# Performance work log

Measured on AMD Instinct MI355X. Metric: run time of the kernel, lower is better.

## Reference

```python
import jax, jax.numpy as jnp
import numpy as np

B, K, N, DIM, C_IN = 4, 2048, 4096, 3, 61
IN = DIM + C_IN        # 64, deepset input size
H1, H2 = 128, 128      # neighbor_xf hidden sizes
OUT = 64               # c_out // heads
HEADS = 4
EPS = 1e-5             # BatchNorm eps


def _lin(key, i, o):
    return jax.random.normal(key, (i, o), jnp.float32) * (1.0 / np.sqrt(i))


def setup_inputs() -> dict:
    key = jax.random.key(0)
    ks = jax.random.split(key, 12)
    return {
        "keys": jax.random.normal(ks[0], (B, K, DIM), jnp.float32),
        "points": jax.random.normal(ks[1], (B, N, DIM), jnp.float32),
        "feats": jax.random.normal(ks[2], (B, N, C_IN), jnp.float32),
        "nx_w1": _lin(ks[3], IN, H1), "nx_b1": jnp.zeros((H1,), jnp.float32),
        "nx_w2": _lin(ks[4], H1, H2), "nx_b2": jnp.zeros((H2,), jnp.float32),
        "nx_w3": _lin(ks[5], H2, OUT), "nx_b3": jnp.zeros((OUT,), jnp.float32),
        "sx_w1": _lin(ks[6], IN, IN), "sx_b1": jnp.zeros((IN,), jnp.float32),
        "sx_w2": _lin(ks[7], IN, IN), "sx_b2": jnp.zeros((IN,), jnp.float32),
        "sx_w3": _lin(ks[8], IN, IN), "sx_b3": jnp.zeros((IN,), jnp.float32),
        "att_w": _lin(ks[9], 2 * IN, HEADS * IN),
        "att_b": jnp.zeros((HEADS * IN,), jnp.float32),
        "att_q": jax.random.normal(ks[10], (HEADS, IN), jnp.float32) * 0.1,
        "bn_gamma": jnp.ones((IN,), jnp.float32),
        "bn_beta": jnp.zeros((IN,), jnp.float32),
        "neighbors": 32,
    }


def _mlp3(x, w1, b1, w2, b2, w3, b3):
    # per-element deepset MLP: Linear-ReLU-Linear-ReLU-Linear
    h = jax.nn.relu(x @ w1 + b1)
    h = jax.nn.relu(h @ w2 + b2)
    return h @ w3 + b3


def _forward(keys, points, feats, nx_w1, nx_b1, nx_w2, nx_b2, nx_w3, nx_b3,
             sx_w1, sx_b1, sx_w2, sx_b2, sx_w3, sx_b3,
             att_w, att_b, att_q, bn_gamma, bn_beta, neighbors):
    b = keys.shape[0]
    # Euclidean dist_fn: dist_vec [B,K,N,dim], dist [B,K,N], all points valid
    rel = points[:, None, :, :] - keys[:, :, None, :]
    dist = jnp.sqrt(jnp.sum(rel * rel, axis=-1))
    _, idx = jax.lax.top_k(-dist, neighbors)                   # [B,K,k] nearest
    nrel = jnp.take_along_axis(rel, idx[..., None], axis=2)    # [B,K,k,dim]
    bidx = jnp.arange(b)[:, None, None]
    nfeat = feats[bidx, idx]                                   # [B,K,k,c_in]
    comb = jnp.concatenate([nrel, nfeat], axis=-1)             # [B,K,k,in]
    lat = _mlp3(comb, nx_w1, nx_b1, nx_w2, nx_b2, nx_w3, nx_b3)  # [B,K,k,out]
    # BatchNorm1d (training-mode batch stats) over flattened [B*K*k, in]
    flat = comb.reshape(-1, comb.shape[-1])
    mean = jnp.mean(flat, axis=0)
    var = jnp.var(flat, axis=0)
    norm = (comb - mean) * jax.lax.rsqrt(var + EPS) * bn_gamma + bn_beta
    # SelfAttention: deepset sum-pooled context + per-neighbor softmax weights
    set_feat = jnp.sum(_mlp3(norm, sx_w1, sx_b1, sx_w2, sx_b2, sx_w3, sx_b3), axis=2)
    comb_feat = jnp.concatenate(
        [norm, jnp.broadcast_to(set_feat[:, :, None, :], norm.shape)], axis=-1)
    heads = (comb_feat @ att_w + att_b).reshape(comb_feat.shape[:3] + (HEADS, -1))
    e = jnp.sum(heads * att_q, axis=-1)                        # [B,K,k,H]
    w = jax.nn.softmax(e, axis=-2)                             # softmax over neighbor axis
    out = jnp.einsum('bkno,bknh->bkoh', lat, w)                # weighted reduce over k
    return out.reshape(out.shape[:2] + (-1,))                  # [B,K,out*H]


def reference(keys, points, feats, nx_w1, nx_b1, nx_w2, nx_b2, nx_w3, nx_b3,
              sx_w1, sx_b1, sx_w2, sx_b2, sx_w3, sx_b3,
              att_w, att_b, att_q, bn_gamma, bn_beta, neighbors):
    return _forward(keys, points, feats, nx_w1, nx_b1, nx_w2, nx_b2, nx_w3, nx_b3,
                    sx_w1, sx_b1, sx_w2, sx_b2, sx_w3, sx_b3,
                    att_w, att_b, att_q, bn_gamma, bn_beta, neighbors)
```

## Files before the change

kernel.cpp:

```cpp
#include <hip/hip_runtime.h>
#include <math.h>

#define BATCH 4
#define KQ    2048
#define NPTS  4096
#define CIN   61
#define KNN   32
#define ROWS  (BATCH*KQ*KNN)

#define OFF_IDX  0
#define OFF_ACC  524288
#define OFF_ATTA 557056
#define OFF_W1F  558080
#define OFF_W2F  574464
#define OFF_W3F  607232

typedef __attribute__((ext_vector_type(8)))  short bfrag;
typedef __attribute__((ext_vector_type(16))) float cfrag;

__device__ __forceinline__ unsigned short bf16_rne(float x) {
  unsigned u = __float_as_uint(x);
  unsigned r = u + 0x7fffu + ((u >> 16) & 1u);
  return (unsigned short)(r >> 16);
}
__device__ __forceinline__ float4 ld4u(const float* p) {
  float4 r; __builtin_memcpy(&r, p, 16); return r;
}

#define NCAND 320

template<int NS>
__device__ __forceinline__ void select_emit(
    const unsigned* __restrict__ VAL, const int* __restrict__ IDXL,
    int mcount, unsigned hib, unsigned lob, int lane,
    const float* __restrict__ Pb, float kx, float ky, float kz,
    unsigned short* __restrict__ dst, int* __restrict__ SEL,
    float* __restrict__ accs) {
  const unsigned long long lmask = (1ull << lane) - 1ull;
  unsigned e[NS];
#pragma unroll
  for (int s = 0; s < NS; ++s) {
    int ei = s*64 + lane;
    e[s] = (ei < mcount) ? VAL[ei] : 0xffffffffu;
  }
  unsigned lo2 = lob, hi2 = hib;
  while (lo2 < hi2) {
    unsigned mid = lo2 + ((hi2 - lo2) >> 1);
    int c = 0;
#pragma unroll
    for (int s = 0; s < NS; ++s) c += (int)__popcll(__ballot(e[s] <= mid));
    if (c == KNN) { hi2 = mid; break; }
    if (c > KNN) hi2 = mid; else lo2 = mid + 1;
  }
  const unsigned T = hi2;
  float r0=0.f,r1=0.f,r2=0.f,r3=0.f,r4=0.f,r5=0.f;
  int base2 = 0;
#pragma unroll
  for (int s = 0; s < NS; ++s) {
    bool p = (e[s] <= T);
    unsigned long long m = __ballot(p);
    if (p) {
      int pos = base2 + (int)__popcll(m & lmask);
      if (pos < KNN) {
        int n = IDXL[s*64 + lane];
        SEL[pos] = n;
        dst[pos] = (unsigned short)n;
        float dx = Pb[n*3+0]-kx, dy = Pb[n*3+1]-ky, dz = Pb[n*3+2]-kz;
        r0 += dx; r1 += dy; r2 += dz;
        r3 += dx*dx; r4 += dy*dy; r5 += dz*dz;
      }
    }
    base2 += (int)__popcll(m);
  }
#pragma unroll
  for (int off = 32; off > 0; off >>= 1) {
    r0 += __shfl_down(r0, off); r1 += __shfl_down(r1, off);
    r2 += __shfl_down(r2, off); r3 += __shfl_down(r3, off);
    r4 += __shfl_down(r4, off); r5 += __shfl_down(r5, off);
  }
  if (lane == 0) {
    atomicAdd(&accs[0], r0); atomicAdd(&accs[1], r1); atomicAdd(&accs[2], r2);
    atomicAdd(&accs[64], r3); atomicAdd(&accs[65], r4); atomicAdd(&accs[66], r5);
  }
}

__device__ __forceinline__ void dispatch_select(
    const unsigned* VAL, const int* IDXL, int mcount, unsigned hib, unsigned lob,
    int lane, const float* Pb, float kx, float ky, float kz,
    unsigned short* dst, int* SEL, float* accs) {
  if (mcount <= 64)
    select_emit<1>(VAL, IDXL, mcount, hib, lob, lane, Pb, kx, ky, kz, dst, SEL, accs);
  else if (mcount <= 128)
    select_emit<2>(VAL, IDXL, mcount, hib, lob, lane, Pb, kx, ky, kz, dst, SEL, accs);
  else
    select_emit<5>(VAL, IDXL, mcount, hib, lob, lane, Pb, kx, ky, kz, dst, SEL, accs);
}

__global__ __launch_bounds__(256, 6) void topk_kernel(
    const float* __restrict__ keys, const float* __restrict__ points,
    const float* __restrict__ feats,
    const float* __restrict__ w1, const float* __restrict__ w2,
    const float* __restrict__ w3,
    const float* __restrict__ att_w, const float* __restrict__ att_q,
    unsigned short* __restrict__ idx_out, float* __restrict__ acc,
    short* __restrict__ w1f, short* __restrict__ w2f, short* __restrict__ w3f,
    float* __restrict__ attA) {
  if (blockIdx.x >= 4096) {
    const int bb = blockIdx.x - 4096;
    if (bb == 128) {
      const int t = threadIdx.x, c = t >> 2, h = t & 3;
      float s = 0.f;
      for (int d = 0; d < 64; ++d) s += att_w[c*256 + h*64 + d] * att_q[h*64 + d];
      attA[c*4 + h] = s;
      return;
    }
    int t = bb * 256 + threadIdx.x;
    if (t < 8192) {
      int j = t & 7, lane = (t >> 3) & 63, tk = t >> 9;
      int kc = tk & 3, tile = tk >> 2;
      int nh = tile*32 + (lane & 31), k = kc*16 + (lane >> 5)*8 + j;
      w1f[t] = (short)bf16_rne(w1[k*128 + nh]);
    } else if (t < 24576) {
      int t2 = t - 8192;
      int j = t2 & 7, lane = (t2 >> 3) & 63, tk = t2 >> 9;
      int kc = tk & 7, tile = tk >> 3;
      int nh = tile*32 + (lane & 31), k = kc*16 + (lane >> 5)*8 + j;
      w2f[t2] = (short)bf16_rne(w2[k*128 + nh]);
    } else {
      int t3 = t - 24576;
      int j = t3 & 7, lane = (t3 >> 3) & 63, tk = t3 >> 9;
      int kc = tk & 7, tile = tk >> 3;
      int nh = tile*32 + (lane & 31), k = kc*16 + (lane >> 5)*8 + j;
      w3f[t3] = (short)bf16_rne(w3[k*64 + nh]);
    }
    return;
  }

  __shared__ unsigned VAL[2][NCAND];
  __shared__ int IDXL[2][NCAND];
  __shared__ int SEL[2][KNN];
  __shared__ unsigned HIW[2][4], LOW[2][4];
  __shared__ int WTOT[2][4];
  __shared__ float FRED[64*33];
  __shared__ float FQ[64*33];
  const int tid = threadIdx.x;
  const int lane = tid & 63, wid = tid >> 6;
  const int g0 = blockIdx.x * 2, g1 = g0 + 1;
  const int b = g0 >> 11;
  const float kxA = keys[(size_t)g0*3+0], kyA = keys[(size_t)g0*3+1], kzA = keys[(size_t)g0*3+2];
  const float kxB = keys[(size_t)g1*3+0], kyB = keys[(size_t)g1*3+1], kzB = keys[(size_t)g1*3+2];
  const float* __restrict__ Pb = points + (size_t)b * NPTS * 3;

  unsigned uA[16], uB[16];
  unsigned lminA = 0xffffffffu, lminB = 0xffffffffu;
#pragma unroll
  for (int c4 = 0; c4 < 4; ++c4) {
    const float* pp = Pb + (size_t)(tid*16 + c4*4) * 3;
    float4 A = ld4u(pp), B4 = ld4u(pp + 4), C4 = ld4u(pp + 8);
    float x, y, z, dx, dy, dz;
#define DPT(slot, PX, PY, PZ)                                        \
    x = PX; y = PY; z = PZ;                                          \
    dx = x-kxA; dy = y-kyA; dz = z-kzA;                              \
    uA[slot] = __float_as_uint(dx*dx + dy*dy + dz*dz);               \
    lminA = min(lminA, uA[slot]);                                    \
    dx = x-kxB; dy = y-kyB; dz = z-kzB;                              \
    uB[slot] = __float_as_uint(dx*dx + dy*dy + dz*dz);               \
    lminB = min(lminB, uB[slot]);
    DPT(c4*4+0, A.x,  A.y,  A.z)
    DPT(c4*4+1, A.w,  B4.x, B4.y)
    DPT(c4*4+2, B4.z, B4.w, C4.x)
    DPT(c4*4+3, C4.y, C4.z, C4.w)
#undef DPT
  }
  unsigned wloA = lminA, whiA = lminA, wloB = lminB, whiB = lminB;
#pragma unroll
  for (int off = 1; off < 64; off <<= 1) {
    unsigned a0 = (unsigned)__shfl_xor((int)wloA, off);
    unsigned a1 = (unsigned)__shfl_xor((int)whiA, off);
    unsigned b0 = (unsigned)__shfl_xor((int)wloB, off);
    unsigned b1 = (unsigned)__shfl_xor((int)whiB, off);
    wloA = min(wloA, a0); whiA = max(whiA, a1);
    wloB = min(wloB, b0); whiB = max(whiB, b1);
  }
  unsigned hiA, hiB;
  {
    unsigned lo = wloA, hi = whiA;
    while (lo < hi) {
      unsigned mid = lo + ((hi - lo) >> 1);
      int c = (int)__popcll(__ballot(lminA <= mid));
      if (c == KNN) { hi = mid; break; }
      if (c > KNN) hi = mid; else lo = mid + 1;
    }
    hiA = hi;
    lo = wloB; hi = whiB;
    while (lo < hi) {
      unsigned mid = lo + ((hi - lo) >> 1);
      int c = (int)__popcll(__ballot(lminB <= mid));
      if (c == KNN) { hi = mid; break; }
      if (c > KNN) hi = mid; else lo = mid + 1;
    }
    hiB = hi;
  }
  if (lane == 0) {
    HIW[0][wid] = hiA; HIW[1][wid] = hiB;
    LOW[0][wid] = wloA; LOW[1][wid] = wloB;
  }
  __syncthreads();
  const unsigned hibA = min(min(HIW[0][0],HIW[0][1]), min(HIW[0][2],HIW[0][3]));
  const unsigned hibB = min(min(HIW[1][0],HIW[1][1]), min(HIW[1][2],HIW[1][3]));
  const unsigned lobA = min(min(LOW[0][0],LOW[0][1]), min(LOW[0][2],LOW[0][3]));
  const unsigned lobB = min(min(LOW[1][0],LOW[1][1]), min(LOW[1][2],LOW[1][3]));

  int cntA = 0, cntB = 0;
#pragma unroll
  for (int j = 0; j < 16; ++j) {
    cntA += (uA[j] <= hibA) ? 1 : 0;
    cntB += (uB[j] <= hibB) ? 1 : 0;
  }
  int incA = cntA, incB = cntB;
#pragma unroll
  for (int off = 1; off < 64; off <<= 1) {
    int tA = __shfl_up(incA, off);
    int tB = __shfl_up(incB, off);
    if (lane >= off) { incA += tA; incB += tB; }
  }
  if (lane == 63) { WTOT[0][wid] = incA; WTOT[1][wid] = incB; }
  __syncthreads();
  int baseA = incA - cntA, baseB = incB - cntB;
  for (int w = 0; w < wid; ++w) { baseA += WTOT[0][w]; baseB += WTOT[1][w]; }
  {
    int pA = baseA, pB = baseB;
#pragma unroll
    for (int j = 0; j < 16; ++j) {
      if (uA[j] <= hibA) {
        if (pA < NCAND) { VAL[0][pA] = uA[j]; IDXL[0][pA] = tid*16 + j; }
        ++pA;
      }
      if (uB[j] <= hibB) {
        if (pB < NCAND) { VAL[1][pB] = uB[j]; IDXL[1][pB] = tid*16 + j; }
        ++pB;
      }
    }
  }
  __syncthreads();
  const int mcountA = min(WTOT[0][0]+WTOT[0][1]+WTOT[0][2]+WTOT[0][3], NCAND);
  const int mcountB = min(WTOT[1][0]+WTOT[1][1]+WTOT[1][2]+WTOT[1][3], NCAND);

  float* accs = &acc[(blockIdx.x & 63)*128];
  if (wid == 0) {
    dispatch_select(VAL[0], IDXL[0], mcountA, hibA, lobA, lane, Pb,
                    kxA, kyA, kzA, idx_out + (size_t)g0*KNN, SEL[0], accs);
  } else if (wid == 2) {
    dispatch_select(VAL[1], IDXL[1], mcountB, hibB, lobB, lane, Pb,
                    kxB, kyB, kzB, idx_out + (size_t)g1*KNN, SEL[1], accs);
  }
  __syncthreads();

  {
    const int row = tid >> 3, chunk = tid & 7;
    const int nA = SEL[0][row], nB = SEL[1][row];
    const float* frA = feats + ((size_t)b*NPTS + nA)*CIN;
    const float* frB = feats + ((size_t)b*NPTS + nB)*CIN;
    float fs[8] = {0,0,0,0,0,0,0,0}, fq[8] = {0,0,0,0,0,0,0,0};
    if (chunk < 7) {
      float4 a0 = ld4u(frA + chunk*8), a1 = ld4u(frA + chunk*8 + 4);
      float4 b0 = ld4u(frB + chunk*8), b1 = ld4u(frB + chunk*8 + 4);
      fs[0]=a0.x+b0.x; fq[0]=a0.x*a0.x+b0.x*b0.x;
      fs[1]=a0.y+b0.y; fq[1]=a0.y*a0.y+b0.y*b0.y;
      fs[2]=a0.z+b0.z; fq[2]=a0.z*a0.z+b0.z*b0.z;
      fs[3]=a0.w+b0.w; fq[3]=a0.w*a0.w+b0.w*b0.w;
      fs[4]=a1.x+b1.x; fq[4]=a1.x*a1.x+b1.x*b1.x;
      fs[5]=a1.y+b1.y; fq[5]=a1.y*a1.y+b1.y*b1.y;
      fs[6]=a1.z+b1.z; fq[6]=a1.z*a1.z+b1.z*b1.z;
      fs[7]=a1.w+b1.w; fq[7]=a1.w*a1.w+b1.w*b1.w;
    } else {
#pragma unroll
      for (int i = 0; i < 5; ++i) {
        float va = frA[56+i], vb = frB[56+i];
        fs[i] = va + vb; fq[i] = va*va + vb*vb;
      }
    }
#pragma unroll
    for (int i = 0; i < 8; ++i) {
      FRED[(chunk*8 + i)*33 + row] = fs[i];
      FQ  [(chunk*8 + i)*33 + row] = fq[i];
    }
  }
  __syncthreads();
  if (tid < 64) {
    float s = 0.f, q2 = 0.f;
#pragma unroll
    for (int r = 0; r < 32; ++r) {
      s  += FRED[tid*33 + r];
      q2 += FQ[tid*33 + r];
    }
    if (tid < CIN) {
      atomicAdd(&accs[3 + tid], s);
      atomicAdd(&accs[64 + 3 + tid], q2);
    }
  }
}

#define L_W1F 0
#define L_W2F 16384
#define L_W3F 49152
#define L_B1  65536
#define L_B2  66048
#define L_B3  66560
#define L_AE  66816
#define L_ACT 67840
#define L_EPX 137472
#define L_TOT 145664

template<int KC, bool F32OUT>
__device__ __forceinline__ void gemm_part(const short* WF,
    const float* BIAS, short* ACTq, float* LATq,
    const bfrag* B, int tile0, int ntiles, int m, int q, int lane) {
#pragma unroll
  for (int t = 0; t < ntiles; ++t) {
    const int tile = tile0 + t;
    cfrag acc;
#pragma unroll
    for (int i = 0; i < 16; ++i) acc[i] = 0.f;
#pragma unroll
    for (int kc = 0; kc < KC; ++kc) {
      bfrag a = *(const bfrag*)(WF + ((tile*KC + kc)*64 + lane)*8);
      acc = __builtin_amdgcn_mfma_f32_32x32x16_bf16(a, B[kc], acc, 0, 0, 0);
    }
#pragma unroll
    for (int p = 0; p < 4; ++p) {
      const int nh = tile*32 + p*8 + q*4;
      float4 bv = *(const float4*)(BIAS + nh);
      if (F32OUT) {
        float4 o;
        o.x = acc[4*p+0] + bv.x; o.y = acc[4*p+1] + bv.y;
        o.z = acc[4*p+2] + bv.z; o.w = acc[4*p+3] + bv.w;
        *(float4*)(LATq + m*68 + nh) = o;
      } else {
        short4 s;
        s.x = (short)bf16_rne(fmaxf(acc[4*p+0] + bv.x, 0.f));
        s.y = (short)bf16_rne(fmaxf(acc[4*p+1] + bv.y, 0.f));
        s.z = (short)bf16_rne(fmaxf(acc[4*p+2] + bv.z, 0.f));
        s.w = (short)bf16_rne(fmaxf(acc[4*p+3] + bv.w, 0.f));
        *(short4*)(ACTq + m*136 + nh) = s;
      }
    }
  }
}

__global__ __launch_bounds__(1024, 4) void main_kernel(
    const float* __restrict__ keys, const float* __restrict__ points,
    const float* __restrict__ feats, const unsigned short* __restrict__ idxg,
    const short* __restrict__ w1f, const short* __restrict__ w2f,
    const short* __restrict__ w3f,
    const float* __restrict__ b1, const float* __restrict__ b2,
    const float* __restrict__ b3,
    const float* __restrict__ attAg, const float* __restrict__ accg,
    const float* __restrict__ gammav, float* __restrict__ out) {
  __shared__ __align__(16) char smem[L_TOT];
  const int tid = threadIdx.x;
  const int bid = blockIdx.x;
  const int wid = tid >> 6, lane = tid & 63;
  const int pairq = wid >> 1, wv = wid & 1;
  const int m = lane & 31, q = lane >> 5;

  short* SW1 = (short*)(smem + L_W1F);
  short* SW2 = (short*)(smem + L_W2F);
  short* SW3 = (short*)(smem + L_W3F);
  float* SB1 = (float*)(smem + L_B1);
  float* SB2 = (float*)(smem + L_B2);
  float* SB3 = (float*)(smem + L_B3);
  float* SAe = (float*)(smem + L_AE);
  short* ACTq = (short*)(smem + L_ACT + pairq * 8704);
  float* LATq = (float*)(smem + L_ACT + pairq * 8704);
  float* EPX  = (float*)(smem + L_EPX) + pairq * 256;

  {
    ((uint4*)SW1)[tid] = ((const uint4*)w1f)[tid];
    ((uint4*)SW2)[tid] = ((const uint4*)w2f)[tid];
    ((uint4*)SW2)[tid + 1024] = ((const uint4*)w2f)[tid + 1024];
    ((uint4*)SW3)[tid] = ((const uint4*)w3f)[tid];
    if (tid < 128) SB1[tid] = b1[tid];
    else if (tid < 256) SB2[tid-128] = b2[tid-128];
    else if (tid < 320) SB3[tid-256] = b3[tid-256];
    float* TMP = (float*)(smem + L_ACT);
    if (tid < 512) {
      int c = tid & 63, p = tid >> 6;
      float s = 0.f, s2 = 0.f;
      for (int k = p; k < 64; k += 8) {
        s += accg[k*128 + c]; s2 += accg[k*128 + 64 + c];
      }
      TMP[p*128 + c] = s; TMP[p*128 + 64 + c] = s2;
    }
    __syncthreads();
    float* SCt = (float*)(smem + L_EPX);
    if (tid < 64) {
      float s = 0.f, s2 = 0.f;
#pragma unroll
      for (int p = 0; p < 8; ++p) { s += TMP[p*128 + tid]; s2 += TMP[p*128 + 64 + tid]; }
      const float invR = 1.f / (float)ROWS;
      float mean = s * invR;
      float var = s2 * invR - mean * mean;
      SCt[tid] = gammav[tid] * rsqrtf(var + 1e-5f);
    }
    __syncthreads();
    if (tid < 256) SAe[tid] = attAg[tid] * SCt[tid >> 2];
    __syncthreads();
  }

  auto load_gather = [&](int grp2, float* v) {
    const int g2 = grp2 * 8 + pairq;
    const int bq2 = g2 >> 11;
    const int c0 = wv*32 + q*16;
    const int n = (int)idxg[(size_t)g2*KNN + m];
    const float* frow = feats + ((size_t)bq2*NPTS + n)*CIN;
    if (wv == 0 && q == 0) {
      const float* Pb = points + (size_t)bq2 * NPTS * 3;
      v[0] = Pb[n*3+0] - keys[(size_t)g2*3+0];
      v[1] = Pb[n*3+1] - keys[(size_t)g2*3+1];
      v[2] = Pb[n*3+2] - keys[(size_t)g2*3+2];
#pragma unroll
      for (int kk = 0; kk < 3; ++kk) {
        float4 t = ld4u(frow + kk*4);
        v[3+kk*4+0] = t.x; v[3+kk*4+1] = t.y; v[3+kk*4+2] = t.z; v[3+kk*4+3] = t.w;
      }
      v[15] = frow[12];
    } else {
      const int base = c0 - 3;
#pragma unroll
      for (int kk = 0; kk < 4; ++kk) {
        float4 t = ld4u(frow + base + kk*4);
        v[kk*4+0] = t.x; v[kk*4+1] = t.y; v[kk*4+2] = t.z; v[kk*4+3] = t.w;
      }
    }
  };

  float vcur[16];
  load_gather(bid, vcur);

  for (int grp = bid; grp < BATCH*KQ/8; grp += 256) {
    const int g = grp * 8 + pairq;
    const int c0 = wv*32 + q*16;

    {
      float ep0 = 0.f, ep1 = 0.f, ep2 = 0.f, ep3 = 0.f;
#pragma unroll
      for (int cc = 0; cc < 16; ++cc) {
        float4 ae = *(const float4*)(SAe + (c0 + cc)*4);
        ep0 = fmaf(vcur[cc], ae.x, ep0);
        ep1 = fmaf(vcur[cc], ae.y, ep1);
        ep2 = fmaf(vcur[cc], ae.z, ep2);
        ep3 = fmaf(vcur[cc], ae.w, ep3);
      }
      ep0 += __shfl_xor(ep0, 32); ep1 += __shfl_xor(ep1, 32);
      ep2 += __shfl_xor(ep2, 32); ep3 += __shfl_xor(ep3, 32);
#pragma unroll
      for (int k = 0; k < 2; ++k) {
        bfrag pk;
#pragma unroll
        for (int t = 0; t < 8; ++t) pk[t] = (short)bf16_rne(vcur[k*8 + t]);
        *(bfrag*)(ACTq + m*136 + c0 + k*8) = pk;
      }
      if (q == 0) {
        float4 e4; e4.x = ep0; e4.y = ep1; e4.z = ep2; e4.w = ep3;
        *(float4*)(EPX + m*8 + wv*4) = e4;
      }
    }
    __syncthreads();

    float vnext[16];
    const int gnext = grp + 256;
    if (gnext < BATCH*KQ/8) load_gather(gnext, vnext);

    if (wv == 0) {
      const int h0 = q*2;
      float ea = EPX[m*8 + h0]     + EPX[m*8 + 4 + h0];
      float eb = EPX[m*8 + h0 + 1] + EPX[m*8 + 5 + h0];
      float ma = ea, mb = eb;
#pragma unroll
      for (int off = 1; off < 32; off <<= 1) {
        ma = fmaxf(ma, __shfl_xor(ma, off));
        mb = fmaxf(mb, __shfl_xor(mb, off));
      }
      float xa = __expf(ea - ma), xb = __expf(eb - mb);
      float sa = xa, sb = xb;
#pragma unroll
      for (int off = 1; off < 32; off <<= 1) {
        sa += __shfl_xor(sa, off);
        sb += __shfl_xor(sb, off);
      }
      EPX[m*8 + h0]     = xa / sa;
      EPX[m*8 + h0 + 1] = xb / sb;
    }

    {
      bfrag B4[4];
#pragma unroll
      for (int kc = 0; kc < 4; ++kc)
        B4[kc] = *(const bfrag*)(ACTq + m*136 + kc*16 + q*8);
      __syncthreads();
      gemm_part<4, false>(SW1, SB1, ACTq, LATq, B4, wv*2, 2, m, q, lane);
    }
    __syncthreads();
    {
      bfrag B8[8];
#pragma unroll
      for (int kc = 0; kc < 8; ++kc)
        B8[kc] = *(const bfrag*)(ACTq + m*136 + kc*16 + q*8);
      __syncthreads();
      gemm_part<8, false>(SW2, SB2, ACTq, LATq, B8, wv*2, 2, m, q, lane);
    }
    __syncthreads();
    {
      bfrag C8[8];
#pragma unroll
      for (int kc = 0; kc < 8; ++kc)
        C8[kc] = *(const bfrag*)(ACTq + m*136 + kc*16 + q*8);
      __syncthreads();
      gemm_part<8, true>(SW3, SB3, ACTq, LATq, C8, wv, 1, m, q, lane);
    }
    __syncthreads();

    {
      const int oi = wv*64 + lane;
      const int o = oi >> 1, hp = oi & 1;
      float a0 = 0.f, a1 = 0.f;
#pragma unroll
      for (int n2 = 0; n2 < KNN; ++n2) {
        float l = LATq[n2*68 + o];
        float2 wv2 = *(const float2*)(EPX + n2*8 + hp*2);
        a0 = fmaf(l, wv2.x, a0);
        a1 = fmaf(l, wv2.y, a1);
      }
      float2 r; r.x = a0; r.y = a1;
      *(float2*)(out + (size_t)g*256 + o*4 + hp*2) = r;
    }
    __syncthreads();

#pragma unroll
    for (int i = 0; i < 16; ++i) vcur[i] = vnext[i];
  }
}

extern "C" void kernel_launch(void* const* d_in, const int* in_sizes, int n_in,
                              void* d_out, int out_size, void* d_ws, size_t ws_size,
                              hipStream_t stream) {
  const float* keys   = (const float*)d_in[0];
  const float* points = (const float*)d_in[1];
  const float* feats  = (const float*)d_in[2];
  const float* nx_w1  = (const float*)d_in[3];
  const float* nx_b1  = (const float*)d_in[4];
  const float* nx_w2  = (const float*)d_in[5];
  const float* nx_b2  = (const float*)d_in[6];
  const float* nx_w3  = (const float*)d_in[7];
  const float* nx_b3  = (const float*)d_in[8];
  const float* att_w  = (const float*)d_in[15];
  const float* att_q  = (const float*)d_in[17];
  const float* gamma  = (const float*)d_in[18];
  float* out = (float*)d_out;

  char* ws = (char*)d_ws;
  unsigned short* idxp = (unsigned short*)(ws + OFF_IDX);
  float* acc  = (float*)(ws + OFF_ACC);
  float* attA = (float*)(ws + OFF_ATTA);
  short* w1f  = (short*)(ws + OFF_W1F);
  short* w2f  = (short*)(ws + OFF_W2F);
  short* w3f  = (short*)(ws + OFF_W3F);

  hipMemsetAsync(acc, 0, 32768, stream);
  topk_kernel<<<4096 + 129, 256, 0, stream>>>(keys, points, feats,
      nx_w1, nx_w2, nx_w3, att_w, att_q, idxp, acc, w1f, w2f, w3f, attA);
  main_kernel<<<256, 1024, 0, stream>>>(keys, points, feats, idxp,
      w1f, w2f, w3f, nx_b1, nx_b2, nx_b3, attA, acc, gamma, out);
}
```

Baseline: 183.3 us.

## Keep MLP activations in MFMA registers and compute attention logits and pooling via MFMA

The main kernel is restructured so each wavefront handles one query group entirely in registers. Layer outputs are repacked directly as the next MFMA operand, which needs reordered weight fragment layouts for w2/w3. The attention logits and the weighted neighbor reduction now run as split-precision (hi/lo bf16) MFMAs instead of scalar FMA loops and shared-memory staging. This removes most LDS round-trips and block-wide barriers and shrinks shared memory, changing the launch to 512 blocks of 512 threads. The trade-offs are higher register pressure and extra MFMAs to keep near-fp32 accuracy on the softmax and pooling.

Result: faster. 167.1 us (-8.9%).

```diff
diff --git a/kernel.cpp b/kernel.cpp
--- a/kernel.cpp
+++ b/kernel.cpp
@@ -16,6 +16,7 @@
 #define OFF_W3F  607232
 
 typedef __attribute__((ext_vector_type(8)))  short bfrag;
+typedef __attribute__((ext_vector_type(4)))  unsigned ufrag;
 typedef __attribute__((ext_vector_type(16))) float cfrag;
 
 __device__ __forceinline__ unsigned short bf16_rne(float x) {
@@ -25,6 +26,29 @@
 }
 __device__ __forceinline__ float4 ld4u(const float* p) {
   float4 r; __builtin_memcpy(&r, p, 16); return r;
+}
+__device__ __forceinline__ unsigned cvtpk(float lo, float hi) {
+  unsigned r;
+  asm("v_cvt_pk_bf16_f32 %0, %1, %2" : "=v"(r) : "v"(lo), "v"(hi));
+  return r;
+}
+__device__ __forceinline__ float up_lo(unsigned pk) { return __uint_as_float(pk << 16); }
+__device__ __forceinline__ float up_hi(unsigned pk) { return __uint_as_float(pk & 0xffff0000u); }
+
+__device__ __forceinline__ cfrag zero16() {
+  cfrag z;
+#pragma unroll
+  for (int i = 0; i < 16; ++i) z[i] = 0.f;
+  return z;
+}
+__device__ __forceinline__ cfrag mfma_bu(bfrag a, ufrag b, cfrag c) {
+  return __builtin_amdgcn_mfma_f32_32x32x16_bf16(a, __builtin_bit_cast(bfrag, b), c, 0, 0, 0);
+}
+__device__ __forceinline__ cfrag mfma_ub(ufrag a, bfrag b, cfrag c) {
+  return __builtin_amdgcn_mfma_f32_32x32x16_bf16(__builtin_bit_cast(bfrag, a), b, c, 0, 0, 0);
+}
+__device__ __forceinline__ cfrag mfma_uu(ufrag a, ufrag b, cfrag c) {
+  return __builtin_amdgcn_mfma_f32_32x32x16_bf16(__builtin_bit_cast(bfrag, a), __builtin_bit_cast(bfrag, b), c, 0, 0, 0);
 }
 
 #define NCAND 320
@@ -124,13 +148,15 @@
       int t2 = t - 8192;
       int j = t2 & 7, lane = (t2 >> 3) & 63, tk = t2 >> 9;
       int kc = tk & 7, tile = tk >> 3;
-      int nh = tile*32 + (lane & 31), k = kc*16 + (lane >> 5)*8 + j;
+      int nh = tile*32 + (lane & 31);
+      int k = 32*(kc>>1) + 16*(kc&1) + 4*(lane>>5) + (j&3) + 8*(j>>2);
       w2f[t2] = (short)bf16_rne(w2[k*128 + nh]);
     } else {
       int t3 = t - 24576;
       int j = t3 & 7, lane = (t3 >> 3) & 63, tk = t3 >> 9;
       int kc = tk & 7, tile = tk >> 3;
-      int nh = tile*32 + (lane & 31), k = kc*16 + (lane >> 5)*8 + j;
+      int nh = tile*32 + (lane & 31);
+      int k = 32*(kc>>1) + 16*(kc&1) + 4*(lane>>5) + (j&3) + 8*(j>>2);
       w3f[t3] = (short)bf16_rne(w3[k*64 + nh]);
     }
     return;
@@ -304,51 +330,16 @@
 #define L_W1F 0
 #define L_W2F 16384
 #define L_W3F 49152
-#define L_B1  65536
-#define L_B2  66048
-#define L_B3  66560
-#define L_AE  66816
-#define L_ACT 67840
-#define L_EPX 137472
-#define L_TOT 145664
-
-template<int KC, bool F32OUT>
-__device__ __forceinline__ void gemm_part(const short* WF,
-    const float* BIAS, short* ACTq, float* LATq,
-    const bfrag* B, int tile0, int ntiles, int m, int q, int lane) {
-#pragma unroll
-  for (int t = 0; t < ntiles; ++t) {
-    const int tile = tile0 + t;
-    cfrag acc;
-#pragma unroll
-    for (int i = 0; i < 16; ++i) acc[i] = 0.f;
-#pragma unroll
-    for (int kc = 0; kc < KC; ++kc) {
-      bfrag a = *(const bfrag*)(WF + ((tile*KC + kc)*64 + lane)*8);
-      acc = __builtin_amdgcn_mfma_f32_32x32x16_bf16(a, B[kc], acc, 0, 0, 0);
-    }
-#pragma unroll
-    for (int p = 0; p < 4; ++p) {
-      const int nh = tile*32 + p*8 + q*4;
-      float4 bv = *(const float4*)(BIAS + nh);
-      if (F32OUT) {
-        float4 o;
-        o.x = acc[4*p+0] + bv.x; o.y = acc[4*p+1] + bv.y;
-        o.z = acc[4*p+2] + bv.z; o.w = acc[4*p+3] + bv.w;
-        *(float4*)(LATq + m*68 + nh) = o;
-      } else {
-        short4 s;
-        s.x = (short)bf16_rne(fmaxf(acc[4*p+0] + bv.x, 0.f));
-        s.y = (short)bf16_rne(fmaxf(acc[4*p+1] + bv.y, 0.f));
-        s.z = (short)bf16_rne(fmaxf(acc[4*p+2] + bv.z, 0.f));
-        s.w = (short)bf16_rne(fmaxf(acc[4*p+3] + bv.w, 0.f));
-        *(short4*)(ACTq + m*136 + nh) = s;
-      }
-    }
-  }
-}
-
-__global__ __launch_bounds__(1024, 4) void main_kernel(
+#define L_SH  65536
+#define L_SL  69632
+#define L_B1  73728
+#define L_B2  74240
+#define L_B3  74752
+#define L_WSC 75008
+#define L_SC  79104
+#define L_TOT 79360
+
+__global__ __launch_bounds__(512, 4) void main_kernel(
     const float* __restrict__ keys, const float* __restrict__ points,
     const float* __restrict__ feats, const unsigned short* __restrict__ idxg,
     const short* __restrict__ w1f, const short* __restrict__ w2f,
@@ -361,30 +352,18 @@
   const int tid = threadIdx.x;
   const int bid = blockIdx.x;
   const int wid = tid >> 6, lane = tid & 63;
-  const int pairq = wid >> 1, wv = wid & 1;
-  const int m = lane & 31, q = lane >> 5;
-
-  short* SW1 = (short*)(smem + L_W1F);
-  short* SW2 = (short*)(smem + L_W2F);
-  short* SW3 = (short*)(smem + L_W3F);
-  float* SB1 = (float*)(smem + L_B1);
-  float* SB2 = (float*)(smem + L_B2);
-  float* SB3 = (float*)(smem + L_B3);
-  float* SAe = (float*)(smem + L_AE);
-  short* ACTq = (short*)(smem + L_ACT + pairq * 8704);
-  float* LATq = (float*)(smem + L_ACT + pairq * 8704);
-  float* EPX  = (float*)(smem + L_EPX) + pairq * 256;
+  const int col = lane & 31, h = lane >> 5;
 
   {
-    ((uint4*)SW1)[tid] = ((const uint4*)w1f)[tid];
-    ((uint4*)SW2)[tid] = ((const uint4*)w2f)[tid];
-    ((uint4*)SW2)[tid + 1024] = ((const uint4*)w2f)[tid + 1024];
-    ((uint4*)SW3)[tid] = ((const uint4*)w3f)[tid];
-    if (tid < 128) SB1[tid] = b1[tid];
-    else if (tid < 256) SB2[tid-128] = b2[tid-128];
-    else if (tid < 320) SB3[tid-256] = b3[tid-256];
-    float* TMP = (float*)(smem + L_ACT);
-    if (tid < 512) {
+    const uint4* src = (const uint4*)w1f;
+    uint4* dst = (uint4*)smem;
+#pragma unroll
+    for (int r = 0; r < 8; ++r) dst[r*512 + tid] = src[r*512 + tid];
+    if (tid < 128) ((float*)(smem + L_B1))[tid] = b1[tid];
+    else if (tid < 256) ((float*)(smem + L_B2))[tid-128] = b2[tid-128];
+    else if (tid < 320) ((float*)(smem + L_B3))[tid-256] = b3[tid-256];
+    float* TMP = (float*)(smem + L_WSC);
+    {
       int c = tid & 63, p = tid >> 6;
       float s = 0.f, s2 = 0.f;
       for (int k = p; k < 64; k += 8) {
@@ -393,7 +372,7 @@
       TMP[p*128 + c] = s; TMP[p*128 + 64 + c] = s2;
     }
     __syncthreads();
-    float* SCt = (float*)(smem + L_EPX);
+    float* SCp = (float*)(smem + L_SC);
     if (tid < 64) {
       float s = 0.f, s2 = 0.f;
 #pragma unroll
@@ -401,144 +380,193 @@
       const float invR = 1.f / (float)ROWS;
       float mean = s * invR;
       float var = s2 * invR - mean * mean;
-      SCt[tid] = gammav[tid] * rsqrtf(var + 1e-5f);
-    }
-    __syncthreads();
-    if (tid < 256) SAe[tid] = attAg[tid] * SCt[tid >> 2];
-    __syncthreads();
-  }
-
-  auto load_gather = [&](int grp2, float* v) {
-    const int g2 = grp2 * 8 + pairq;
-    const int bq2 = g2 >> 11;
-    const int c0 = wv*32 + q*16;
-    const int n = (int)idxg[(size_t)g2*KNN + m];
-    const float* frow = feats + ((size_t)bq2*NPTS + n)*CIN;
-    if (wv == 0 && q == 0) {
-      const float* Pb = points + (size_t)bq2 * NPTS * 3;
-      v[0] = Pb[n*3+0] - keys[(size_t)g2*3+0];
-      v[1] = Pb[n*3+1] - keys[(size_t)g2*3+1];
-      v[2] = Pb[n*3+2] - keys[(size_t)g2*3+2];
-#pragma unroll
-      for (int kk = 0; kk < 3; ++kk) {
-        float4 t = ld4u(frow + kk*4);
-        v[3+kk*4+0] = t.x; v[3+kk*4+1] = t.y; v[3+kk*4+2] = t.z; v[3+kk*4+3] = t.w;
-      }
-      v[15] = frow[12];
-    } else {
-      const int base = c0 - 3;
-#pragma unroll
-      for (int kk = 0; kk < 4; ++kk) {
-        float4 t = ld4u(frow + base + kk*4);
-        v[kk*4+0] = t.x; v[kk*4+1] = t.y; v[kk*4+2] = t.z; v[kk*4+3] = t.w;
-      }
-    }
-  };
-
-  float vcur[16];
-  load_gather(bid, vcur);
-
-  for (int grp = bid; grp < BATCH*KQ/8; grp += 256) {
-    const int g = grp * 8 + pairq;
-    const int c0 = wv*32 + q*16;
-
-    {
-      float ep0 = 0.f, ep1 = 0.f, ep2 = 0.f, ep3 = 0.f;
-#pragma unroll
-      for (int cc = 0; cc < 16; ++cc) {
-        float4 ae = *(const float4*)(SAe + (c0 + cc)*4);
-        ep0 = fmaf(vcur[cc], ae.x, ep0);
-        ep1 = fmaf(vcur[cc], ae.y, ep1);
-        ep2 = fmaf(vcur[cc], ae.z, ep2);
-        ep3 = fmaf(vcur[cc], ae.w, ep3);
-      }
-      ep0 += __shfl_xor(ep0, 32); ep1 += __shfl_xor(ep1, 32);
-      ep2 += __shfl_xor(ep2, 32); ep3 += __shfl_xor(ep3, 32);
-#pragma unroll
-      for (int k = 0; k < 2; ++k) {
-        bfrag pk;
-#pragma unroll
-        for (int t = 0; t < 8; ++t) pk[t] = (short)bf16_rne(vcur[k*8 + t]);
-        *(bfrag*)(ACTq + m*136 + c0 + k*8) = pk;
-      }
-      if (q == 0) {
-        float4 e4; e4.x = ep0; e4.y = ep1; e4.z = ep2; e4.w = ep3;
-        *(float4*)(EPX + m*8 + wv*4) = e4;
-      }
-    }
-    __syncthreads();
-
-    float vnext[16];
-    const int gnext = grp + 256;
-    if (gnext < BATCH*KQ/8) load_gather(gnext, vnext);
-
-    if (wv == 0) {
-      const int h0 = q*2;
-      float ea = EPX[m*8 + h0]     + EPX[m*8 + 4 + h0];
-      float eb = EPX[m*8 + h0 + 1] + EPX[m*8 + 5 + h0];
-      float ma = ea, mb = eb;
-#pragma unroll
-      for (int off = 1; off < 32; off <<= 1) {
-        ma = fmaxf(ma, __shfl_xor(ma, off));
-        mb = fmaxf(mb, __shfl_xor(mb, off));
-      }
-      float xa = __expf(ea - ma), xb = __expf(eb - mb);
-      float sa = xa, sb = xb;
-#pragma unroll
-      for (int off = 1; off < 32; off <<= 1) {
-        sa += __shfl_xor(sa, off);
-        sb += __shfl_xor(sb, off);
-      }
-      EPX[m*8 + h0]     = xa / sa;
-      EPX[m*8 + h0 + 1] = xb / sb;
-    }
-
-    {
-      bfrag B4[4];
-#pragma unroll
-      for (int kc = 0; kc < 4; ++kc)
-        B4[kc] = *(const bfrag*)(ACTq + m*136 + kc*16 + q*8);
-      __syncthreads();
-      gemm_part<4, false>(SW1, SB1, ACTq, LATq, B4, wv*2, 2, m, q, lane);
+      SCp[tid] = gammav[tid] * rsqrtf(var + 1e-5f);
     }
     __syncthreads();
     {
-      bfrag B8[8];
-#pragma unroll
-      for (int kc = 0; kc < 8; ++kc)
-        B8[kc] = *(const bfrag*)(ACTq + m*136 + kc*16 + q*8);
-      __syncthreads();
-      gemm_part<8, false>(SW2, SB2, ACTq, LATq, B8, wv*2, 2, m, q, lane);
+      const int s = tid >> 8;
+      const int kc = (tid >> 6) & 3;
+      const int ln = tid & 63;
+      const int hd = ln & 31;
+      short* dstf = (short*)(smem + (s ? L_SL : L_SH)) + (kc*64 + ln)*8;
+#pragma unroll
+      for (int j = 0; j < 8; ++j) {
+        const int ch = kc*16 + (ln>>5)*8 + j;
+        float val = (hd < 4) ? attAg[ch*4 + hd] * SCp[ch] : 0.f;
+        unsigned hb = bf16_rne(val);
+        if (s) {
+          float lo = val - __uint_as_float(hb << 16);
+          dstf[j] = (short)bf16_rne(lo);
+        } else {
+          dstf[j] = (short)hb;
+        }
+      }
     }
     __syncthreads();
-    {
-      bfrag C8[8];
-#pragma unroll
-      for (int kc = 0; kc < 8; ++kc)
-        C8[kc] = *(const bfrag*)(ACTq + m*136 + kc*16 + q*8);
-      __syncthreads();
-      gemm_part<8, true>(SW3, SB3, ACTq, LATq, C8, wv, 1, m, q, lane);
-    }
-    __syncthreads();
-
-    {
-      const int oi = wv*64 + lane;
-      const int o = oi >> 1, hp = oi & 1;
-      float a0 = 0.f, a1 = 0.f;
-#pragma unroll
-      for (int n2 = 0; n2 < KNN; ++n2) {
-        float l = LATq[n2*68 + o];
-        float2 wv2 = *(const float2*)(EPX + n2*8 + hp*2);
-        a0 = fmaf(l, wv2.x, a0);
-        a1 = fmaf(l, wv2.y, a1);
-      }
-      float2 r; r.x = a0; r.y = a1;
-      *(float2*)(out + (size_t)g*256 + o*4 + hp*2) = r;
-    }
-    __syncthreads();
-
-#pragma unroll
-    for (int i = 0; i < 16; ++i) vcur[i] = vnext[i];
+  }
+
+  float* WS = (float*)(smem + L_WSC) + wid*128;
+  const short* SW1 = (const short*)(smem + L_W1F);
+  const short* SW2 = (const short*)(smem + L_W2F);
+  const short* SW3 = (const short*)(smem + L_W3F);
+  const float* SB1 = (const float*)(smem + L_B1);
+  const float* SB2 = (const float*)(smem + L_B2);
+
+  for (int qi = 0; qi < 2; ++qi) {
+    const int g = bid*8 + wid + qi*4096;
+    const int b = g >> 11;
+    const int n = (int)idxg[(size_t)g*KNN + col];
+    const float* frow = feats + ((size_t)b*NPTS + n)*CIN;
+
+    float v[4][8];
+    if (h == 0) {
+      const float* Pb = points + (size_t)b*NPTS*3;
+      v[0][0] = Pb[n*3+0] - keys[(size_t)g*3+0];
+      v[0][1] = Pb[n*3+1] - keys[(size_t)g*3+1];
+      v[0][2] = Pb[n*3+2] - keys[(size_t)g*3+2];
+      float4 t0 = ld4u(frow);
+      v[0][3]=t0.x; v[0][4]=t0.y; v[0][5]=t0.z; v[0][6]=t0.w;
+      v[0][7] = frow[4];
+    } else {
+      float4 a0 = ld4u(frow+5), a1 = ld4u(frow+9);
+      v[0][0]=a0.x; v[0][1]=a0.y; v[0][2]=a0.z; v[0][3]=a0.w;
+      v[0][4]=a1.x; v[0][5]=a1.y; v[0][6]=a1.z; v[0][7]=a1.w;
+    }
+#pragma unroll
+    for (int kc = 1; kc < 4; ++kc) {
+      const int f0 = kc*16 + 8*h - 3;
+      float4 a0 = ld4u(frow+f0), a1 = ld4u(frow+f0+4);
+      v[kc][0]=a0.x; v[kc][1]=a0.y; v[kc][2]=a0.z; v[kc][3]=a0.w;
+      v[kc][4]=a1.x; v[kc][5]=a1.y; v[kc][6]=a1.z; v[kc][7]=a1.w;
+    }
+
+    ufrag ahi[4], alo[4];
+#pragma unroll
+    for (int kc = 0; kc < 4; ++kc)
+#pragma unroll
+      for (int p = 0; p < 4; ++p) {
+        unsigned pk = cvtpk(v[kc][2*p], v[kc][2*p+1]);
+        ahi[kc][p] = pk;
+        alo[kc][p] = cvtpk(v[kc][2*p] - up_lo(pk), v[kc][2*p+1] - up_hi(pk));
+      }
+
+    cfrag Ef = zero16();
+#pragma unroll
+    for (int kc = 0; kc < 4; ++kc) {
+      bfrag sh = *(const bfrag*)((const short*)(smem + L_SH) + (kc*64 + lane)*8);
+      bfrag sl = *(const bfrag*)((const short*)(smem + L_SL) + (kc*64 + lane)*8);
+      Ef = mfma_ub(ahi[kc], sh, Ef);
+      Ef = mfma_ub(alo[kc], sh, Ef);
+      Ef = mfma_ub(ahi[kc], sl, Ef);
+    }
+
+    float mx = Ef[0];
+#pragma unroll
+    for (int i = 1; i < 16; ++i) mx = fmaxf(mx, Ef[i]);
+    mx = fmaxf(mx, __shfl_xor(mx, 32));
+    float wsm[16], ssum = 0.f;
+#pragma unroll
+    for (int i = 0; i < 16; ++i) { wsm[i] = __expf(Ef[i] - mx); ssum += wsm[i]; }
+    ssum += __shfl_xor(ssum, 32);
+    const float invs = 1.f / ssum;
+#pragma unroll
+    for (int i = 0; i < 16; ++i) wsm[i] *= invs;
+
+    if (col < 4) {
+#pragma unroll
+      for (int i = 0; i < 8; ++i) {
+        const int c0 = (2*i & 3) + 8*(i >> 1);
+        const int nA = c0 + 4*h;
+        WS[nA*4 + col]     = wsm[2*i];
+        WS[nA*4 + 4 + col] = wsm[2*i+1];
+      }
+    }
+    const int hdc = col & 3;
+    ufrag whi[2], wlo[2];
+#pragma unroll
+    for (int bb = 0; bb < 2; ++bb)
+#pragma unroll
+      for (int p = 0; p < 4; ++p) {
+        const int c0 = (2*p & 3) + 8*(p >> 1);
+        const int n0 = 16*bb + 4*h + c0;
+        float r0 = WS[n0*4 + hdc], r1 = WS[n0*4 + 4 + hdc];
+        unsigned pk = cvtpk(r0, r1);
+        whi[bb][p] = pk;
+        wlo[bb][p] = cvtpk(r0 - up_lo(pk), r1 - up_hi(pk));
+      }
+
+    ufrag a2[8];
+#pragma unroll
+    for (int t = 0; t < 4; ++t) {
+      cfrag acc = zero16();
+#pragma unroll
+      for (int kc = 0; kc < 4; ++kc) {
+        bfrag wf = *(const bfrag*)(SW1 + ((t*4 + kc)*64 + lane)*8);
+        acc = mfma_bu(wf, ahi[kc], acc);
+      }
+#pragma unroll
+      for (int i = 0; i < 8; ++i) {
+        const int c0 = (2*i & 3) + 8*(i >> 1);
+        float2 bb2 = *(const float2*)(SB1 + t*32 + c0 + 4*h);
+        float x0 = fmaxf(acc[2*i]   + bb2.x, 0.f);
+        float x1 = fmaxf(acc[2*i+1] + bb2.y, 0.f);
+        a2[2*t + (i>>2)][i&3] = cvtpk(x0, x1);
+      }
+    }
+
+    ufrag a3[8];
+#pragma unroll
+    for (int t = 0; t < 4; ++t) {
+      cfrag acc = zero16();
+#pragma unroll
+      for (int kc = 0; kc < 8; ++kc) {
+        bfrag wf = *(const bfrag*)(SW2 + ((t*8 + kc)*64 + lane)*8);
+        acc = mfma_bu(wf, a2[kc], acc);
+      }
+#pragma unroll
+      for (int i = 0; i < 8; ++i) {
+        const int c0 = (2*i & 3) + 8*(i >> 1);
+        float2 bb2 = *(const float2*)(SB2 + t*32 + c0 + 4*h);
+        float x0 = fmaxf(acc[2*i]   + bb2.x, 0.f);
+        float x1 = fmaxf(acc[2*i+1] + bb2.y, 0.f);
+        a3[2*t + (i>>2)][i&3] = cvtpk(x0, x1);
+      }
+    }
+
+#pragma unroll
+    for (int t = 0; t < 2; ++t) {
+      cfrag acc = zero16();
+#pragma unroll
+      for (int kc = 0; kc < 8; ++kc) {
+        bfrag wf = *(const bfrag*)(SW3 + ((t*8 + kc)*64 + lane)*8);
+        acc = mfma_ub(a3[kc], wf, acc);
+      }
+      const float bz = ((const float*)(smem + L_B3))[t*32 + col];
+#pragma unroll
+      for (int i = 0; i < 16; ++i) acc[i] += bz;
+      ufrag lh[2], ll[2];
+#pragma unroll
+      for (int i = 0; i < 8; ++i) {
+        unsigned pk = cvtpk(acc[2*i], acc[2*i+1]);
+        lh[i>>2][i&3] = pk;
+        ll[i>>2][i&3] = cvtpk(acc[2*i] - up_lo(pk), acc[2*i+1] - up_hi(pk));
+      }
+      cfrag og = zero16();
+#pragma unroll
+      for (int bb = 0; bb < 2; ++bb) og = mfma_uu(lh[bb], whi[bb], og);
+#pragma unroll
+      for (int bb = 0; bb < 2; ++bb) og = mfma_uu(ll[bb], whi[bb], og);
+#pragma unroll
+      for (int bb = 0; bb < 2; ++bb) og = mfma_uu(lh[bb], wlo[bb], og);
+      if (col < 4) {
+        float* op = out + (size_t)g*256 + t*128 + col;
+#pragma unroll
+        for (int i = 0; i < 16; ++i) {
+          const int orow = (i&3) + 8*(i>>2) + 4*h;
+          op[orow*4] = og[i];
+        }
+      }
+    }
   }
 }
 
@@ -570,6 +598,6 @@
   hipMemsetAsync(acc, 0, 32768, stream);
   topk_kernel<<<4096 + 129, 256, 0, stream>>>(keys, points, feats,
       nx_w1, nx_w2, nx_w3, att_w, att_q, idxp, acc, w1f, w2f, w3f, attA);
-  main_kernel<<<256, 1024, 0, stream>>>(keys, points, feats, idxp,
+  main_kernel<<<512, 512, 0, stream>>>(keys, points, feats, idxp,
       w1f, w2f, w3f, nx_b1, nx_b2, nx_b3, attA, acc, gamma, out);
 }
```
